# Kernel optimization log

Hardware: AMD Instinct MI355X
Metric: run time of the kernel (lower is better)

The kernel has to match this reference:

```python
import jax, jax.numpy as jnp
import numpy as np

TEMP = 1.0  # composition softmax temperature

def _bank_topk(x, U, V, logits, top_k):
    # softmax over primitive logits, select top-k, renormalize, fused low-rank projection
    w = jax.nn.softmax(logits / TEMP)                     # [P]
    tw, ti = jax.lax.top_k(w, top_k)                      # [k], [k]
    tw = tw / tw.sum()
    Us = U[ti]                                            # [k, d_in, r]
    Vs = V[ti]                                            # [k, r, d_out]
    h = jnp.einsum('bsd,kdr->bksr', x, Us)                # low-rank bottleneck
    return jnp.einsum('bksr,kro,k->bso', h, Vs, tw)       # weighted fuse

def reference(x, q_U, q_V, k_U, k_V, v_U, v_V, q_logits, k_logits, v_logits, out_w, top_k):
    B, S, _ = x.shape
    H, D = 16, 64
    q = _bank_topk(x, q_U, q_V, q_logits, top_k)
    k = _bank_topk(x, k_U, k_V, k_logits, top_k)
    v = _bank_topk(x, v_U, v_V, v_logits, top_k)
    q = q.reshape(B, S, H, D).transpose(0, 2, 1, 3)       # [B,H,S,D]
    k = k.reshape(B, S, H, D).transpose(0, 2, 1, 3)
    v = v.reshape(B, S, H, D).transpose(0, 2, 1, 3)
    scale = 1.0 / jnp.sqrt(jnp.asarray(D, dtype=x.dtype))
    scores = jnp.einsum('bhqd,bhkd->bhqk', q, k) * scale  # [B,H,S,S]
    causal = jnp.triu(jnp.ones((S, S), dtype=bool), 1)
    scores = jnp.where(causal[None, None], jnp.finfo(x.dtype).min, scores)
    probs = jax.nn.softmax(scores, axis=-1)
    out = jnp.einsum('bhqk,bhkd->bhqd', probs, v)
    out = out.transpose(0, 2, 1, 3).reshape(B, S, H * D)
    return out @ out_w.T                                   # nn.Linear(H*D, d_model, bias=False)

def setup_inputs() -> dict:
    key = jax.random.key(0)
    ks = jax.random.split(key, 11)
    P, d, r = 16, 1024, 64
    B, S = 4, 1024
    f = jnp.float32
    inp = {
        'x': jax.random.normal(ks[0], (B, S, d), f),
        'q_U': jax.random.normal(ks[1], (P, d, r), f) * (1.0 / np.sqrt(d)),
        'q_V': jax.random.normal(ks[2], (P, r, d), f) * (1.0 / np.sqrt(r)),
        'k_U': jax.random.normal(ks[3], (P, d, r), f) * (1.0 / np.sqrt(d)),
        'k_V': jax.random.normal(ks[4], (P, r, d), f) * (1.0 / np.sqrt(r)),
        'v_U': jax.random.normal(ks[5], (P, d, r), f) * (1.0 / np.sqrt(d)),
        'v_V': jax.random.normal(ks[6], (P, r, d), f) * (1.0 / np.sqrt(r)),
        'q_logits': jax.random.normal(ks[7], (P,), f) * 0.01,
        'k_logits': jax.random.normal(ks[8], (P,), f) * 0.01,
        'v_logits': jax.random.normal(ks[9], (P,), f) * 0.01,
        'out_w': jax.random.normal(ks[10], (d, d), f) * (1.0 / np.sqrt(d)),
        'top_k': 4,
    }
    return inp
```

## Files before the change

kernel.cpp:

```cpp
#include <hip/hip_runtime.h>
#include <math.h>

#define D_MODEL 1024
#define RANK    64
#define PMAX    16
#define S_LEN   1024
#define HD      64
#define MROWS   4096
#define NHEAD   16
#define BATCH   4
#define KCMAX   (PMAX * RANK)

typedef short short8v __attribute__((ext_vector_type(8)));
typedef short short4v __attribute__((ext_vector_type(4)));
typedef float floatx4 __attribute__((ext_vector_type(4)));

typedef __attribute__((address_space(1))) const unsigned int* gptr_t;
typedef __attribute__((address_space(3))) unsigned int* lptr_t;
typedef __attribute__((address_space(3))) short* lds3s;

static __device__ __forceinline__ void async16(const void* g, void* l) {
    __builtin_amdgcn_global_load_lds((gptr_t)g, (lptr_t)l, 16, 0, 0);
}

static __device__ __forceinline__ short f2bf(float f) {
    unsigned int u = __float_as_uint(f);
    u = (u + 0x7fffu + ((u >> 16) & 1u)) >> 16;
    return (short)u;
}

__global__ __launch_bounds__(256) void convert_bf16_kernel(
    const float* __restrict__ x, short* __restrict__ xb,
    const float* __restrict__ w, short* __restrict__ wb) {
    int i = blockIdx.x * 256 + threadIdx.x;
    const int NX = MROWS * D_MODEL / 4;
    const int NW = D_MODEL * D_MODEL / 4;
    const float* src;
    short* dst;
    if (i < NX) {
        src = x; dst = xb;
    } else {
        i -= NX;
        if (i >= NW) return;
        src = w; dst = wb;
    }
    float4 f = ((const float4*)src)[i];
    short4 o;
    o.x = f2bf(f.x); o.y = f2bf(f.y); o.z = f2bf(f.z); o.w = f2bf(f.w);
    ((short4*)dst)[i] = o;
}

__global__ __launch_bounds__(256) void prep_uv_kernel(
    const float* __restrict__ qU, const float* __restrict__ kU,
    const float* __restrict__ vU,
    const float* __restrict__ qV, const float* __restrict__ kV,
    const float* __restrict__ vV,
    const float* __restrict__ ql, const float* __restrict__ kl,
    const float* __restrict__ vl,
    const int* __restrict__ topk,
    short* __restrict__ Uc, short* __restrict__ Vt) {
    int z    = blockIdx.z;
    int j    = blockIdx.y;
    int tile = blockIdx.x;
    int t    = threadIdx.x;
    int K = *topk; if (K < 1) K = 1; if (K > PMAX) K = PMAX;
    if (j >= K) return;
    __shared__ float T[64][65];
    int bank = (z < 3) ? z : z - 3;

    const float* lg = (bank == 0) ? ql : (bank == 1) ? kl : vl;
    float l[PMAX];
    bool used[PMAX];
    for (int i = 0; i < PMAX; ++i) { l[i] = lg[i]; used[i] = false; }
    int   si[PMAX];
    float sl[PMAX];
    for (int jj = 0; jj < K; ++jj) {
        int best = -1; float bv = -INFINITY;
        for (int i = 0; i < PMAX; ++i)
            if (!used[i] && l[i] > bv) { bv = l[i]; best = i; }
        used[best] = true; si[jj] = best; sl[jj] = bv;
    }
    float mx = sl[0], sum = 0.f, ej = 0.f;
    for (int jj = 0; jj < K; ++jj) {
        float e = __expf(sl[jj] - mx);
        sum += e;
        if (jj == j) ej = e;
    }
    int   p  = si[j];
    float wj = ej / sum;

    if (z < 3) {
        const float* U = (bank == 0) ? qU : (bank == 1) ? kU : vU;
        const float* src = U + (size_t)p * D_MODEL * RANK;
        short* dst = Uc + (size_t)bank * D_MODEL * KCMAX;
        int r4 = (t & 15) * 4;
        int dl = t >> 4;
#pragma unroll
        for (int i = 0; i < 4; ++i) {
            int d = tile * 64 + i * 16 + dl;
            float4 f = *(const float4*)&src[(size_t)d * RANK + r4];
            short4 o;
            o.x = f2bf(f.x); o.y = f2bf(f.y); o.z = f2bf(f.z); o.w = f2bf(f.w);
            *(short4*)&dst[(size_t)d * KCMAX + j * 64 + r4] = o;
        }
    } else {
        const float* V = (bank == 0) ? qV : (bank == 1) ? kV : vV;
        const float* src = V + (size_t)p * RANK * D_MODEL;
        int n0 = tile * 64;
        int nl = t & 63, rq = t >> 6;
#pragma unroll
        for (int i = 0; i < 16; ++i) {
            int rl = i * 4 + rq;
            T[nl][rl] = src[(size_t)rl * D_MODEL + n0 + nl] * wj;
        }
        __syncthreads();
        short* dst = Vt + (size_t)bank * D_MODEL * KCMAX;
        int rr = t >> 2;
#pragma unroll
        for (int i = 0; i < 4; ++i) {
            int c = (t & 3) * 16 + i * 4;
            short4 o;
            o.x = f2bf(T[rr][c + 0]); o.y = f2bf(T[rr][c + 1]);
            o.z = f2bf(T[rr][c + 2]); o.w = f2bf(T[rr][c + 3]);
            *(short4*)&dst[(size_t)(n0 + rr) * KCMAX + j * 64 + c] = o;
        }
    }
}

static __device__ __forceinline__ void mfma_gemm_tile(
    const short* __restrict__ A, const short* __restrict__ B, int kl,
    int lda, int ldb, int m0, int n0, short* As, short* Bs, floatx4 acc[4][4]) {
    const int t    = threadIdx.x;
    const int w    = t >> 6;
    const int lane = t & 63;
    const int wm   = w & 1, wn = w >> 1;
    const int colL = lane & 15, quad = lane >> 4;
    const int srow  = lane >> 2;
    const int skoff = (lane & 3) * 8;

#pragma unroll
    for (int i = 0; i < 4; ++i)
#pragma unroll
        for (int j = 0; j < 4; ++j) acc[i][j] = (floatx4){0.f, 0.f, 0.f, 0.f};

    for (int k0 = 0; k0 < kl; k0 += 32) {
        async16(A + (size_t)(m0 + w * 16 + srow) * lda + k0 + skoff,
                As + (w * 16 + srow) * 32 + skoff);
        async16(A + (size_t)(m0 + 64 + w * 16 + srow) * lda + k0 + skoff,
                As + (64 + w * 16 + srow) * 32 + skoff);
        async16(B + (size_t)(n0 + w * 16 + srow) * ldb + k0 + skoff,
                Bs + (w * 16 + srow) * 32 + skoff);
        async16(B + (size_t)(n0 + 64 + w * 16 + srow) * ldb + k0 + skoff,
                Bs + (64 + w * 16 + srow) * 32 + skoff);
        __syncthreads();
        short8v af[4], bf[4];
#pragma unroll
        for (int i = 0; i < 4; ++i)
            af[i] = *(const short8v*)&As[(wm * 64 + i * 16 + colL) * 32 + quad * 8];
#pragma unroll
        for (int j = 0; j < 4; ++j)
            bf[j] = *(const short8v*)&Bs[(wn * 64 + j * 16 + colL) * 32 + quad * 8];
#pragma unroll
        for (int i = 0; i < 4; ++i)
#pragma unroll
            for (int j = 0; j < 4; ++j)
                acc[i][j] = __builtin_amdgcn_mfma_f32_16x16x32_bf16(af[i], bf[j], acc[i][j], 0, 0, 0);
        __syncthreads();
    }
}

__global__ __launch_bounds__(256) void gemm_weff_kernel(
    const short* __restrict__ Vt, const short* __restrict__ Uc,
    const int* __restrict__ topk, short* __restrict__ Wt) {
    int K = *topk; if (K < 1) K = 1; if (K > PMAX) K = PMAX;
    int id = blockIdx.x + 8 * (blockIdx.y + 8 * blockIdx.z);
    int sw = (id & 7) * 24 + (id >> 3);
    int m0 = (sw & 7) * 128; int rest = sw >> 3;
    int n0 = (rest & 7) * 128; int bank = rest >> 3;
    __shared__ short As[128 * 32];
    __shared__ short Bs[128 * 32];
    floatx4 acc[4][4];
    mfma_gemm_tile(Vt + (size_t)bank * D_MODEL * KCMAX,
                   Uc + (size_t)bank * D_MODEL * KCMAX,
                   K * 64, KCMAX, KCMAX, m0, n0, As, Bs, acc);

    const int t = threadIdx.x, w = t >> 6, lane = t & 63;
    const int wm = w & 1, wn = w >> 1, colL = lane & 15, quad = lane >> 4;
    short* Wb = Wt + (size_t)bank * D_MODEL * D_MODEL;
#pragma unroll
    for (int i = 0; i < 4; ++i)
#pragma unroll
        for (int j = 0; j < 4; ++j)
#pragma unroll
            for (int r = 0; r < 4; ++r)
                Wb[(size_t)(m0 + wm * 64 + i * 16 + quad * 4 + r) * D_MODEL +
                   (n0 + wn * 64 + j * 16 + colL)] = f2bf(acc[i][j][r]);
}

__global__ __launch_bounds__(256) void gemm_qkv_kernel(
    const short* __restrict__ xb, const short* __restrict__ Wt,
    short* __restrict__ qkv) {
    int id = blockIdx.x + 32 * (blockIdx.y + 8 * blockIdx.z);
    int sw = (id & 7) * 96 + (id >> 3);
    int m0 = (sw & 31) * 128; int rest = sw >> 5;
    int n0 = (rest & 7) * 128; int bank = rest >> 3;
    __shared__ short As[128 * 32];
    __shared__ short Bs[128 * 32];
    floatx4 acc[4][4];
    mfma_gemm_tile(xb, Wt + (size_t)bank * D_MODEL * D_MODEL,
                   D_MODEL, D_MODEL, D_MODEL, m0, n0, As, Bs, acc);

    const int t = threadIdx.x, w = t >> 6, lane = t & 63;
    const int wm = w & 1, wn = w >> 1, colL = lane & 15, quad = lane >> 4;
    short* outp = qkv + (size_t)bank * MROWS * D_MODEL;
#pragma unroll
    for (int i = 0; i < 4; ++i)
#pragma unroll
        for (int j = 0; j < 4; ++j)
#pragma unroll
            for (int r = 0; r < 4; ++r) {
                int m = m0 + wm * 64 + i * 16 + quad * 4 + r;
                int n = n0 + wn * 64 + j * 16 + colL;
                int b = m >> 10, s = m & 1023;
                int head = n >> 6, d = n & 63;
                outp[(((size_t)(b * NHEAD + head) << 10) + s) * HD + d] = f2bf(acc[i][j][r]);
            }
}

__global__ __launch_bounds__(256) void gemm_proj_kernel(
    const short* __restrict__ attnb, const short* __restrict__ wb,
    float* __restrict__ outp) {
    int id = blockIdx.x + 32 * blockIdx.y;
    int sw = (id & 7) * 32 + (id >> 3);
    int m0 = (sw & 31) * 128;
    int n0 = (sw >> 5) * 128;
    __shared__ short As[128 * 32];
    __shared__ short Bs[128 * 32];
    floatx4 acc[4][4];
    mfma_gemm_tile(attnb, wb, D_MODEL, D_MODEL, D_MODEL, m0, n0, As, Bs, acc);

    const int t = threadIdx.x, w = t >> 6, lane = t & 63;
    const int wm = w & 1, wn = w >> 1, colL = lane & 15, quad = lane >> 4;
#pragma unroll
    for (int i = 0; i < 4; ++i)
#pragma unroll
        for (int j = 0; j < 4; ++j)
#pragma unroll
            for (int r = 0; r < 4; ++r)
                outp[(size_t)(m0 + wm * 64 + i * 16 + quad * 4 + r) * D_MODEL +
                     (n0 + wn * 64 + j * 16 + colL)] = acc[i][j][r];
}

__global__ __launch_bounds__(256) void attn_mfma_kernel(
    const short* __restrict__ qkv,
    short* __restrict__ attn_out) {
    const int t    = threadIdx.x;
    const int w    = t >> 6;
    const int lane = t & 63;
    const int col  = lane & 15;
    const int quad = lane >> 4;
    int id = blockIdx.x + 8 * blockIdx.y;
    int swz = (id & 7) * 64 + (id >> 3);
    const int pr = swz & 7;
    const int bh = swz >> 3;
    const size_t HS   = (size_t)S_LEN * HD;
    const size_t BSTR = (size_t)MROWS * D_MODEL;
    const short* Qg = qkv + (size_t)bh * HS;
    const short* Kg = qkv + BSTR + (size_t)bh * HS;
    const short* Vg = qkv + 2 * BSTR + (size_t)bh * HS;

    __shared__ short Ks[2][128 * 64];
    __shared__ short Vs[2][128 * 64];

    const float SC = 0.125f * 1.44269504f;

    int krow[4], kslot[4], vkey[4], voff[4];
#pragma unroll
    for (int it = 0; it < 4; ++it) {
        int c = t + it * 256;
        krow[it]  = c >> 3;
        kslot[it] = (c & 7) ^ ((c >> 3) & 7);
        int h = c & 1, kr = (c >> 1) & 3, k4 = (c >> 3) & 31, d16 = c >> 8;
        vkey[it] = k4 * 4 + kr;
        voff[it] = d16 * 16 + h * 8;
    }
    const int sw0 = (quad ^ (col & 7)) * 16;
    const int sw1 = ((4 + quad) ^ (col & 7)) * 16;
    lds3s vb = (lds3s)&Vs[0][quad * 64 + col * 4];

    auto STAGE = [&](int buf, int jt) {
#pragma unroll
        for (int it = 0; it < 4; ++it) {
            async16(Kg + (size_t)(jt * 128 + krow[it]) * HD + kslot[it] * 8,
                    &Ks[buf][(t + it * 256) * 8]);
            async16(Vg + (size_t)(jt * 128 + vkey[it]) * HD + voff[it],
                    &Vs[buf][(t + it * 256) * 8]);
        }
    };

    for (int ph = 0; ph < 2; ++ph) {
        const int qt = ph ? (15 - pr) : pr;
        const int qb = qt * 4 + w;
        const int qrow = qt * 64 + w * 16 + col;
        short8v aq0 = *(const short8v*)(Qg + (size_t)qrow * HD + quad * 8);
        short8v aq1 = *(const short8v*)(Qg + (size_t)qrow * HD + 32 + quad * 8);
        asm volatile("s_waitcnt vmcnt(0)" : "+v"(aq0), "+v"(aq1) :: "memory");
        floatx4 O0 = {0.f, 0.f, 0.f, 0.f}, O1 = O0, O2 = O0, O3 = O0;
        float mrow = -INFINITY, lrow = 0.f;
        const int nkv = (qt + 2) >> 1;

        STAGE(0, 0);
        int cur = 0;
        for (int jt = 0; jt < nkv; ++jt) {
            __builtin_amdgcn_sched_barrier(0);
            if (jt + 1 < nkv) {
                STAGE(cur ^ 1, jt + 1);
                asm volatile("s_waitcnt vmcnt(8)" ::: "memory");
            } else {
                asm volatile("s_waitcnt vmcnt(0)" ::: "memory");
            }
            __builtin_amdgcn_s_barrier();
            __builtin_amdgcn_sched_barrier(0);

            const short* Kb = &Ks[cur][0];
            lds3s vbc = vb + cur * (128 * 64);

            const int base = jt * 8;
            float s[8][4];
#pragma unroll
            for (int mb = 0; mb < 8; ++mb) {
                int rel = qb - (base + mb);
                if (rel >= 0) {
                    floatx4 c4 = {0.f, 0.f, 0.f, 0.f};
                    const char* kp = (const char*)Kb + mb * 2048 + col * 128;
                    short8v a0 = *(const short8v*)(kp + sw0);
                    short8v a1 = *(const short8v*)(kp + sw1);
                    c4 = __builtin_amdgcn_mfma_f32_16x16x32_bf16(a0, aq0, c4, 0, 0, 0);
                    c4 = __builtin_amdgcn_mfma_f32_16x16x32_bf16(a1, aq1, c4, 0, 0, 0);
#pragma unroll
                    for (int r = 0; r < 4; ++r) {
                        float v = c4[r] * SC;
                        if (rel == 0 && quad * 4 + r > col) v = -INFINITY;
                        s[mb][r] = v;
                    }
                } else {
#pragma unroll
                    for (int r = 0; r < 4; ++r) s[mb][r] = -INFINITY;
                }
            }
            float tm = -INFINITY;
#pragma unroll
            for (int mb = 0; mb < 8; ++mb)
#pragma unroll
                for (int r = 0; r < 4; ++r) tm = fmaxf(tm, s[mb][r]);
            tm = fmaxf(tm, __shfl_xor(tm, 16));
            tm = fmaxf(tm, __shfl_xor(tm, 32));
            if (__any(tm > mrow + 8.0f)) {
                float mnew  = fmaxf(mrow, tm);
                float alpha = exp2f(mrow - mnew);
                lrow *= alpha;
                mrow = mnew;
#pragma unroll
                for (int r = 0; r < 4; ++r) {
                    float ar = __shfl(alpha, quad * 4 + r);
                    O0[r] *= ar; O1[r] *= ar; O2[r] *= ar; O3[r] *= ar;
                }
            }
            float p[8][4];
            float ps = 0.f;
#pragma unroll
            for (int mb = 0; mb < 8; ++mb)
#pragma unroll
                for (int r = 0; r < 4; ++r) {
                    float e = exp2f(s[mb][r] - mrow);
                    p[mb][r] = e; ps += e;
                }
            ps += __shfl_xor(ps, 16);
            ps += __shfl_xor(ps, 32);
            lrow += ps;

            int lim = qb * 16 + 15 - (jt << 7);
            int ksm = lim >> 5; if (ksm > 3) ksm = 3;
#pragma unroll
            for (int ks = 0; ks < 4; ++ks) {
                if (ks <= ksm) {
                    lds3s vc = vbc + ks * 512;
                    short4v t00, t01, t10, t11, t20, t21, t30, t31;
                    asm volatile("ds_read_b64_tr_b16 %0, %1" : "=v"(t00) : "v"(vc));
                    asm volatile("ds_read_b64_tr_b16 %0, %1" : "=v"(t01) : "v"(vc + 256));
                    asm volatile("ds_read_b64_tr_b16 %0, %1" : "=v"(t10) : "v"(vc + 2048));
                    asm volatile("ds_read_b64_tr_b16 %0, %1" : "=v"(t11) : "v"(vc + 2304));
                    asm volatile("ds_read_b64_tr_b16 %0, %1" : "=v"(t20) : "v"(vc + 4096));
                    asm volatile("ds_read_b64_tr_b16 %0, %1" : "=v"(t21) : "v"(vc + 4352));
                    asm volatile("ds_read_b64_tr_b16 %0, %1" : "=v"(t30) : "v"(vc + 6144));
                    asm volatile("ds_read_b64_tr_b16 %0, %1" : "=v"(t31) : "v"(vc + 6400));
                    short8v ap;
                    ap[0] = f2bf(p[2 * ks][0]);     ap[1] = f2bf(p[2 * ks][1]);
                    ap[2] = f2bf(p[2 * ks][2]);     ap[3] = f2bf(p[2 * ks][3]);
                    ap[4] = f2bf(p[2 * ks + 1][0]); ap[5] = f2bf(p[2 * ks + 1][1]);
                    ap[6] = f2bf(p[2 * ks + 1][2]); ap[7] = f2bf(p[2 * ks + 1][3]);
                    asm volatile("s_waitcnt lgkmcnt(0)" ::: "memory");
                    __builtin_amdgcn_sched_barrier(0);
                    short8v bv0 = __builtin_shufflevector(t00, t01, 0, 1, 2, 3, 4, 5, 6, 7);
                    short8v bv1 = __builtin_shufflevector(t10, t11, 0, 1, 2, 3, 4, 5, 6, 7);
                    short8v bv2 = __builtin_shufflevector(t20, t21, 0, 1, 2, 3, 4, 5, 6, 7);
                    short8v bv3 = __builtin_shufflevector(t30, t31, 0, 1, 2, 3, 4, 5, 6, 7);
                    O0 = __builtin_amdgcn_mfma_f32_16x16x32_bf16(ap, bv0, O0, 0, 0, 0);
                    O1 = __builtin_amdgcn_mfma_f32_16x16x32_bf16(ap, bv1, O1, 0, 0, 0);
                    O2 = __builtin_amdgcn_mfma_f32_16x16x32_bf16(ap, bv2, O2, 0, 0, 0);
                    O3 = __builtin_amdgcn_mfma_f32_16x16x32_bf16(ap, bv3, O3, 0, 0, 0);
                }
            }
            __builtin_amdgcn_sched_barrier(0);
            __builtin_amdgcn_s_barrier();
            cur ^= 1;
        }
        const int b  = bh >> 4;
        const int hh = bh & 15;
        short* orow = attn_out +
            ((size_t)(b * S_LEN) + qt * 64 + w * 16) * D_MODEL + hh * 64;
        float linv = 1.f / lrow;
#pragma unroll
        for (int r = 0; r < 4; ++r) {
            float inv = __shfl(linv, quad * 4 + r);
            short* prw = orow + (size_t)(quad * 4 + r) * D_MODEL;
            prw[0  + col] = f2bf(O0[r] * inv);
            prw[16 + col] = f2bf(O1[r] * inv);
            prw[32 + col] = f2bf(O2[r] * inv);
            prw[48 + col] = f2bf(O3[r] * inv);
        }
    }
}

extern "C" void kernel_launch(void* const* d_in, const int* in_sizes, int n_in,
                              void* d_out, int out_size, void* d_ws, size_t ws_size,
                              hipStream_t stream) {
    const float* x    = (const float*)d_in[0];
    const float* qU   = (const float*)d_in[1];
    const float* qV   = (const float*)d_in[2];
    const float* kU   = (const float*)d_in[3];
    const float* kV   = (const float*)d_in[4];
    const float* vU   = (const float*)d_in[5];
    const float* vV   = (const float*)d_in[6];
    const float* qlg  = (const float*)d_in[7];
    const float* klg  = (const float*)d_in[8];
    const float* vlg  = (const float*)d_in[9];
    const float* outw = (const float*)d_in[10];
    const int*   topk = (const int*)d_in[11];
    float* outp = (float*)d_out;

    char* ws = (char*)d_ws;
    short* xb   = (short*)(ws + 512);
    short* Uc   = xb + (size_t)MROWS * D_MODEL;
    short* Vt   = Uc + (size_t)3 * D_MODEL * KCMAX;
    short* wb   = Vt + (size_t)3 * D_MODEL * KCMAX;
    short* Wt   = wb + (size_t)D_MODEL * D_MODEL;
    short* qkvb = Wt + (size_t)3 * D_MODEL * D_MODEL;
    short* attnb = qkvb + (size_t)3 * MROWS * D_MODEL;

    const int NCV = (MROWS * D_MODEL + D_MODEL * D_MODEL) / 4 / 256;
    convert_bf16_kernel<<<NCV, 256, 0, stream>>>(x, xb, outw, wb);
    prep_uv_kernel<<<dim3(16, 16, 6), 256, 0, stream>>>(
        qU, kU, vU, qV, kV, vV, qlg, klg, vlg, topk, Uc, Vt);
    gemm_weff_kernel<<<dim3(8, 8, 3), 256, 0, stream>>>(Vt, Uc, topk, Wt);
    gemm_qkv_kernel<<<dim3(32, 8, 3), 256, 0, stream>>>(xb, Wt, qkvb);
    attn_mfma_kernel<<<dim3(8, 64), 256, 0, stream>>>(qkvb, attnb);
    gemm_proj_kernel<<<dim3(32, 8), 256, 0, stream>>>(attnb, wb, outp);
}
```

Baseline: 227.8 us.

## Use 128x64 tiles for output projection and single-buffer attention K/V staging

The output projection GEMM switches to a 128x64 tile helper with a doubled grid, aiming to fill more compute units. The attention kernel replaces double-buffered asynchronous K/V staging with a single LDS buffer guarded by block barriers, halving LDS use to allow more resident blocks. This gives up overlap of global loads with compute in attention, and smaller proj tiles reduce data reuse per block.

```diff
diff --git a/kernel.cpp b/kernel.cpp
--- a/kernel.cpp
+++ b/kernel.cpp
@@ -169,6 +169,43 @@
     }
 }
 
+static __device__ __forceinline__ void mfma_gemm_tile_n64(
+    const short* __restrict__ A, const short* __restrict__ B, int kl,
+    int lda, int ldb, int m0, int n0, short* As , short* Bs ,
+    floatx4 acc[2][4]) {
+    const int t    = threadIdx.x;
+    const int w    = t >> 6;
+    const int lane = t & 63;
+    const int colL = lane & 15, quad = lane >> 4;
+    const int row  = t >> 2;
+    const int koff = (t & 3) * 8;
+
+#pragma unroll
+    for (int i = 0; i < 2; ++i)
+#pragma unroll
+        for (int j = 0; j < 4; ++j) acc[i][j] = (floatx4){0.f, 0.f, 0.f, 0.f};
+
+    for (int k0 = 0; k0 < kl; k0 += 32) {
+        async16(A + (size_t)(m0 + row) * lda + k0 + koff,       As + t * 8);
+        async16(A + (size_t)(m0 + 64 + row) * lda + k0 + koff,  As + (t + 256) * 8);
+        async16(B + (size_t)(n0 + row) * ldb + k0 + koff,       Bs + t * 8);
+        __syncthreads();
+        short8v af[2], bf[4];
+#pragma unroll
+        for (int i = 0; i < 2; ++i)
+            af[i] = *(const short8v*)&As[(w * 32 + i * 16 + colL) * 32 + quad * 8];
+#pragma unroll
+        for (int j = 0; j < 4; ++j)
+            bf[j] = *(const short8v*)&Bs[(j * 16 + colL) * 32 + quad * 8];
+#pragma unroll
+        for (int i = 0; i < 2; ++i)
+#pragma unroll
+            for (int j = 0; j < 4; ++j)
+                acc[i][j] = __builtin_amdgcn_mfma_f32_16x16x32_bf16(af[i], bf[j], acc[i][j], 0, 0, 0);
+        __syncthreads();
+    }
+}
+
 __global__ __launch_bounds__(256) void gemm_weff_kernel(
     const short* __restrict__ Vt, const short* __restrict__ Uc,
     const int* __restrict__ topk, short* __restrict__ Wt) {
@@ -231,24 +268,24 @@
     const short* __restrict__ attnb, const short* __restrict__ wb,
     float* __restrict__ outp) {
     int id = blockIdx.x + 32 * blockIdx.y;
-    int sw = (id & 7) * 32 + (id >> 3);
+    int sw = (id & 7) * 64 + (id >> 3);
     int m0 = (sw & 31) * 128;
-    int n0 = (sw >> 5) * 128;
+    int n0 = (sw >> 5) * 64;
     __shared__ short As[128 * 32];
-    __shared__ short Bs[128 * 32];
-    floatx4 acc[4][4];
-    mfma_gemm_tile(attnb, wb, D_MODEL, D_MODEL, D_MODEL, m0, n0, As, Bs, acc);
+    __shared__ short Bs[64 * 32];
+    floatx4 acc[2][4];
+    mfma_gemm_tile_n64(attnb, wb, D_MODEL, D_MODEL, D_MODEL, m0, n0, As, Bs, acc);
 
     const int t = threadIdx.x, w = t >> 6, lane = t & 63;
-    const int wm = w & 1, wn = w >> 1, colL = lane & 15, quad = lane >> 4;
-#pragma unroll
-    for (int i = 0; i < 4; ++i)
+    const int colL = lane & 15, quad = lane >> 4;
+#pragma unroll
+    for (int i = 0; i < 2; ++i)
 #pragma unroll
         for (int j = 0; j < 4; ++j)
 #pragma unroll
             for (int r = 0; r < 4; ++r)
-                outp[(size_t)(m0 + wm * 64 + i * 16 + quad * 4 + r) * D_MODEL +
-                     (n0 + wn * 64 + j * 16 + colL)] = acc[i][j][r];
+                outp[(size_t)(m0 + w * 32 + i * 16 + quad * 4 + r) * D_MODEL +
+                     (n0 + j * 16 + colL)] = acc[i][j][r];
 }
 
 __global__ __launch_bounds__(256) void attn_mfma_kernel(
@@ -269,8 +306,8 @@
     const short* Kg = qkv + BSTR + (size_t)bh * HS;
     const short* Vg = qkv + 2 * BSTR + (size_t)bh * HS;
 
-    __shared__ short Ks[2][128 * 64];
-    __shared__ short Vs[2][128 * 64];
+    __shared__ short Ks[128 * 64];
+    __shared__ short Vs[128 * 64];
 
     const float SC = 0.125f * 1.44269504f;
 
@@ -286,17 +323,7 @@
     }
     const int sw0 = (quad ^ (col & 7)) * 16;
     const int sw1 = ((4 + quad) ^ (col & 7)) * 16;
-    lds3s vb = (lds3s)&Vs[0][quad * 64 + col * 4];
-
-    auto STAGE = [&](int buf, int jt) {
-#pragma unroll
-        for (int it = 0; it < 4; ++it) {
-            async16(Kg + (size_t)(jt * 128 + krow[it]) * HD + kslot[it] * 8,
-                    &Ks[buf][(t + it * 256) * 8]);
-            async16(Vg + (size_t)(jt * 128 + vkey[it]) * HD + voff[it],
-                    &Vs[buf][(t + it * 256) * 8]);
-        }
-    };
+    lds3s vb = (lds3s)&Vs[quad * 64 + col * 4];
 
     for (int ph = 0; ph < 2; ++ph) {
         const int qt = ph ? (15 - pr) : pr;
@@ -304,26 +331,20 @@
         const int qrow = qt * 64 + w * 16 + col;
         short8v aq0 = *(const short8v*)(Qg + (size_t)qrow * HD + quad * 8);
         short8v aq1 = *(const short8v*)(Qg + (size_t)qrow * HD + 32 + quad * 8);
-        asm volatile("s_waitcnt vmcnt(0)" : "+v"(aq0), "+v"(aq1) :: "memory");
         floatx4 O0 = {0.f, 0.f, 0.f, 0.f}, O1 = O0, O2 = O0, O3 = O0;
         float mrow = -INFINITY, lrow = 0.f;
         const int nkv = (qt + 2) >> 1;
 
-        STAGE(0, 0);
-        int cur = 0;
         for (int jt = 0; jt < nkv; ++jt) {
-            __builtin_amdgcn_sched_barrier(0);
-            if (jt + 1 < nkv) {
-                STAGE(cur ^ 1, jt + 1);
-                asm volatile("s_waitcnt vmcnt(8)" ::: "memory");
-            } else {
-                asm volatile("s_waitcnt vmcnt(0)" ::: "memory");
+            __syncthreads();
+#pragma unroll
+            for (int it = 0; it < 4; ++it) {
+                async16(Kg + (size_t)(jt * 128 + krow[it]) * HD + kslot[it] * 8,
+                        Ks + (t + it * 256) * 8);
+                async16(Vg + (size_t)(jt * 128 + vkey[it]) * HD + voff[it],
+                        Vs + (t + it * 256) * 8);
             }
-            __builtin_amdgcn_s_barrier();
-            __builtin_amdgcn_sched_barrier(0);
-
-            const short* Kb = &Ks[cur][0];
-            lds3s vbc = vb + cur * (128 * 64);
+            __syncthreads();
 
             const int base = jt * 8;
             float s[8][4];
@@ -332,7 +353,7 @@
                 int rel = qb - (base + mb);
                 if (rel >= 0) {
                     floatx4 c4 = {0.f, 0.f, 0.f, 0.f};
-                    const char* kp = (const char*)Kb + mb * 2048 + col * 128;
+                    const char* kp = (const char*)Ks + mb * 2048 + col * 128;
                     short8v a0 = *(const short8v*)(kp + sw0);
                     short8v a1 = *(const short8v*)(kp + sw1);
                     c4 = __builtin_amdgcn_mfma_f32_16x16x32_bf16(a0, aq0, c4, 0, 0, 0);
@@ -384,7 +405,7 @@
 #pragma unroll
             for (int ks = 0; ks < 4; ++ks) {
                 if (ks <= ksm) {
-                    lds3s vc = vbc + ks * 512;
+                    lds3s vc = vb + ks * 512;
                     short4v t00, t01, t10, t11, t20, t21, t30, t31;
                     asm volatile("ds_read_b64_tr_b16 %0, %1" : "=v"(t00) : "v"(vc));
                     asm volatile("ds_read_b64_tr_b16 %0, %1" : "=v"(t01) : "v"(vc + 256));
@@ -411,9 +432,6 @@
                     O3 = __builtin_amdgcn_mfma_f32_16x16x32_bf16(ap, bv3, O3, 0, 0, 0);
                 }
             }
-            __builtin_amdgcn_sched_barrier(0);
-            __builtin_amdgcn_s_barrier();
-            cur ^= 1;
         }
         const int b  = bh >> 4;
         const int hh = bh & 15;
@@ -465,5 +483,5 @@
     gemm_weff_kernel<<<dim3(8, 8, 3), 256, 0, stream>>>(Vt, Uc, topk, Wt);
     gemm_qkv_kernel<<<dim3(32, 8, 3), 256, 0, stream>>>(xb, Wt, qkvb);
     attn_mfma_kernel<<<dim3(8, 64), 256, 0, stream>>>(qkvb, attnb);
-    gemm_proj_kernel<<<dim3(32, 8), 256, 0, stream>>>(attnb, wb, outp);
-}
+    gemm_proj_kernel<<<dim3(32, 16), 256, 0, stream>>>(attnb, wb, outp);
+}
```

New measurement: 222.2 us. 2.5% less time.
